# Performance work log

Measured on AMD Instinct MI355X. Metric: run time of the kernel, lower is better.

The kernel has to match this reference:

```python
import jax, jax.numpy as jnp
import numpy as np

KS = (3, 3)   # kernel_size
ST = (1, 1)   # stride
PD = (1, 1)   # padding
EPS = 1e-5


def unfold(x):
    """im2col matching torch.nn.Unfold: [B,C,H,W] -> [B, C*kh*kw, L] with (c,kh,kw) channel order, L row-major."""
    kh, kw = KS; sh, sw = ST; ph, pw = PD
    x = jnp.pad(x, ((0, 0), (0, 0), (ph, ph), (pw, pw)))
    B, C, H, W = x.shape
    Ho = (H - kh) // sh + 1
    Wo = (W - kw) // sw + 1
    I = (jnp.arange(Ho) * sh)[:, None, None, None] + jnp.arange(kh)[None, :, None, None]
    J = (jnp.arange(Wo) * sw)[None, None, :, None] + jnp.arange(kw)[None, None, None, :]
    p = x[:, :, I, J]  # [B, C, Ho, kh, Wo, kw]
    return p.transpose(0, 1, 3, 5, 2, 4).reshape(B, C * kh * kw, Ho * Wo)


def fold(cols, x_shape):
    """torch.nn.Fold is exactly the adjoint of Unfold (overlap-add)."""
    _, vjp = jax.vjp(unfold, jnp.zeros(x_shape, cols.dtype))
    return vjp(cols)[0]


def setup_inputs() -> dict:
    key = jax.random.key(0)
    k = jax.random.split(key, 6)
    B, C, H, W = 16, 64, 64, 64
    Cout, K = 64, KS[0] * KS[1]
    return {
        "x_mag": jax.random.uniform(k[0], (B, C, H, W), jnp.float32),
        "x_ang": jax.random.normal(k[1], (B, C, H, W), jnp.float32),
        "w_mag": jax.random.uniform(k[2], (C, K), jnp.float32),
        "w_ang": jax.random.uniform(k[3], (C, K), jnp.float32),
        "w1": jax.random.uniform(k[4], (C, K), jnp.float32),
        "w2": jax.random.uniform(k[5], (Cout, C), jnp.float32),
    }


def reference(x_mag, x_ang, w_mag, w_ang, w1, w2):
    B, C, H, W = x_mag.shape
    K = KS[0] * KS[1]
    Cout = w2.shape[0]
    Ho = (H + 2 * PD[0] - KS[0]) // ST[0] + 1
    Wo = (W + 2 * PD[1] - KS[1]) // ST[1] + 1

    # outer layer: unfold, mix with normalized weights, fold back (overlap-add)
    nws_mag = w_mag ** 2 / jnp.sum(w_mag ** 2)   # _normalize_weights_squared
    nw_ang = w_ang / jnp.sum(w_ang ** 2)         # _normalize_weights
    cm = unfold(x_mag).reshape(B, C, K, -1) + nws_mag[None, :, :, None]
    ca = unfold(x_ang).reshape(B, C, K, -1) * nw_ang[None, :, :, None]
    fm = fold(cm.reshape(B, C * K, -1), (B, C, H, W))
    fa = fold(ca.reshape(B, C * K, -1), (B, C, H, W))

    # helper: second unfold + weighted Frechet-mean reduction
    tbm = unfold(fm).reshape(B, C, K, -1)  # [B,C,K,L]
    tba = unfold(fa).reshape(B, C, K, -1)
    wmm1 = w1 ** 2 / jnp.sum(w1 ** 2, axis=1, keepdims=True)  # row-normalized
    wmm2 = w2 ** 2 / jnp.sum(w2 ** 2, axis=1, keepdims=True)
    wma1 = w1 ** 2 / jnp.sum(w1 ** 2)                          # globally normalized
    wma2 = w2 ** 2 / jnp.sum(w2 ** 2)

    m1 = jnp.einsum('bckl,ck->bcl', jnp.log(tbm + EPS), wmm1)
    out_mag = jnp.exp(jnp.einsum('bcl,oc->bol', m1, wmm2)).reshape(B, Cout, Ho, Wo)
    a1 = jnp.einsum('bckl,ck->bcl', tba, wma1)
    out_ang = jnp.einsum('bcl,oc->bol', a1, wma2).reshape(B, Cout, Ho, Wo)

    # from_polar -> stack (real, imag) on axis 1
    return jnp.stack([out_mag * jnp.cos(out_ang), out_mag * jnp.sin(out_ang)], axis=1)
```

## Files before the change

### kernel.cpp

```cpp
#include <hip/hip_runtime.h>
#include <math.h>

#define NB 16
#define NC 64
#define NL 4096
#define EPSF 1e-5f
#define LOG_EPSF -11.512925464970229f

#define WS_W2T   0
#define WS_RHO   4096
#define WS_CLS   4160
#define WS_WQ2   5312

#define FMA16(ACC, MV, W) \
  (ACC)[0].x = fmaf((MV).x,(W).x,(ACC)[0].x); (ACC)[0].y = fmaf((MV).y,(W).x,(ACC)[0].y); \
  (ACC)[0].z = fmaf((MV).z,(W).x,(ACC)[0].z); (ACC)[0].w = fmaf((MV).w,(W).x,(ACC)[0].w); \
  (ACC)[1].x = fmaf((MV).x,(W).y,(ACC)[1].x); (ACC)[1].y = fmaf((MV).y,(W).y,(ACC)[1].y); \
  (ACC)[1].z = fmaf((MV).z,(W).y,(ACC)[1].z); (ACC)[1].w = fmaf((MV).w,(W).y,(ACC)[1].w); \
  (ACC)[2].x = fmaf((MV).x,(W).z,(ACC)[2].x); (ACC)[2].y = fmaf((MV).y,(W).z,(ACC)[2].y); \
  (ACC)[2].z = fmaf((MV).z,(W).z,(ACC)[2].z); (ACC)[2].w = fmaf((MV).w,(W).z,(ACC)[2].w); \
  (ACC)[3].x = fmaf((MV).x,(W).w,(ACC)[3].x); (ACC)[3].y = fmaf((MV).y,(W).w,(ACC)[3].y); \
  (ACC)[3].z = fmaf((MV).z,(W).w,(ACC)[3].z); (ACC)[3].w = fmaf((MV).w,(W).w,(ACC)[3].w);

__global__ __launch_bounds__(256) void prep_kernel(
    const float* __restrict__ wm, const float* __restrict__ wa,
    const float* __restrict__ w1, const float* __restrict__ w2,
    float* __restrict__ ws)
{
    __shared__ float r2s[64];
    __shared__ float red[3][4];
    const int tid  = threadIdx.x;
    const int lane = tid & 63;
    const int wv   = tid >> 6;

    if (tid < 64) {
        float s = 0.f;
        for (int c = 0; c < 64; ++c) { float v = w2[tid * 64 + c]; s = fmaf(v, v, s); }
        r2s[tid] = s;
    }
    float p0 = 0.f, p1 = 0.f, p2 = 0.f;
    {
        float v;
        v = wm[tid]; p0 += v * v;  v = wm[tid + 256]; p0 += v * v;
        v = wa[tid]; p1 += v * v;  v = wa[tid + 256]; p1 += v * v;
        v = w1[tid]; p2 += v * v;  v = w1[tid + 256]; p2 += v * v;
        if (tid < 64) {
            v = wm[tid + 512]; p0 += v * v;
            v = wa[tid + 512]; p1 += v * v;
            v = w1[tid + 512]; p2 += v * v;
        }
    }
    #pragma unroll
    for (int s = 32; s; s >>= 1) {
        p0 += __shfl_down(p0, s); p1 += __shfl_down(p1, s); p2 += __shfl_down(p2, s);
    }
    if (lane == 0) { red[0][wv] = p0; red[1][wv] = p1; red[2][wv] = p2; }
    __syncthreads();
    const float s_wm2 = red[0][0] + red[0][1] + red[0][2] + red[0][3];
    const float s_wa2 = red[1][0] + red[1][1] + red[1][2] + red[1][3];
    const float s_w12 = red[2][0] + red[2][1] + red[2][2] + red[2][3];

    const int c0 = blockIdx.x * 4;
    {
        int c = c0 + (tid >> 6), o = tid & 63;
        float v = w2[o * 64 + c];
        ws[WS_W2T + c * 64 + o] = v * v / r2s[o];
    }

    if (blockIdx.x == 0) {
        if (tid < 64) {
            float s22 = 0.f;
            #pragma unroll
            for (int o = 0; o < 64; ++o) s22 += r2s[o];
            ws[WS_RHO + tid] = r2s[tid] / s22;

            const int c = tid;
            float nm[9], na[9];
            const float inv_m = 1.f / s_wm2, inv_a = 1.f / s_wa2;
            #pragma unroll
            for (int k = 0; k < 9; ++k) {
                float v = wm[c * 9 + k];
                nm[k] = v * v * inv_m;
                na[k] = wa[c * 9 + k] * inv_a;
            }
            #pragma unroll
            for (int ci_ = 0; ci_ < 3; ++ci_) {
                #pragma unroll
                for (int cj = 0; cj < 3; ++cj) {
                    float sm = 0.f, sa = 0.f;
                    #pragma unroll
                    for (int ki = 0; ki < 3; ++ki) {
                        bool vi = (ci_ == 0) ? (ki < 2) : ((ci_ == 2) ? (ki > 0) : true);
                        if (!vi) continue;
                        #pragma unroll
                        for (int kj = 0; kj < 3; ++kj) {
                            bool vj = (cj == 0) ? (kj < 2) : ((cj == 2) ? (kj > 0) : true);
                            if (!vj) continue;
                            sm += nm[ki * 3 + kj];
                            sa += na[ki * 3 + kj];
                        }
                    }
                    ws[WS_CLS + c * 9 + ci_ * 3 + cj] = sm;
                    ws[WS_CLS + 576 + c * 9 + ci_ * 3 + cj] = sa;
                }
            }
            float q[9]; float r1c = 0.f;
            #pragma unroll
            for (int k = 0; k < 9; ++k) { float v = w1[c * 9 + k]; q[k] = v * v; r1c += q[k]; }
            const float inv_r = 1.f / r1c, inv_s = 1.f / s_w12;
            #pragma unroll
            for (int k = 0; k < 9; ++k) {
                ws[WS_WQ2 + c * 18 + 2 * k]     = q[k] * inv_r;
                ws[WS_WQ2 + c * 18 + 2 * k + 1] = q[k] * inv_s;
            }
        }
    }
}

__global__ __launch_bounds__(256, 4) void fused_kernel(
    const float* __restrict__ x_mag, const float* __restrict__ x_ang,
    const float* __restrict__ ws, float* __restrict__ out)
{
    __shared__ float m1all[64][64];
    __shared__ float a1all[64][64];

    const int tid  = threadIdx.x;
    const int lane = tid & 63;
    const int wv   = tid >> 6;

    const int bid = (blockIdx.x & 7) * 128 + (blockIdx.x >> 3);
    const int b  = bid >> 6;
    const int iy = bid & 63;

    const int ir0 = iy - 1, ir2 = iy + 1;
    const bool ok0 = (ir0 >= 0), ok2 = (ir2 < 64);
    const int ci0 = (ir0 == 0) ? 0 : 1;
    const int ci1 = (iy == 0) ? 0 : ((iy == 63) ? 2 : 1);
    const int ci2 = (ir2 == 63) ? 2 : 1;
    const int ro0 = ok0 ? ir0 * 64 : 0;
    const int ro1 = iy * 64;
    const int ro2 = ok2 ? ir2 * 64 : 0;

    const bool e0  = (lane == 0);
    const bool e63 = (lane == 63);
    const bool edge = e0 | e63;

    const int cbase = wv * 16;
    const float* xmb = x_mag + ((size_t)(b * NC + cbase) * NL) + lane;
    const float* xab = x_ang + ((size_t)(b * NC + cbase) * NL) + lane;

    float pm[2][3], pa[2][3];
    {
        pm[0][0] = xmb[ro0]; pm[0][1] = xmb[ro1]; pm[0][2] = xmb[ro2];
        pa[0][0] = xab[ro0]; pa[0][1] = xab[ro1]; pa[0][2] = xab[ro2];
        pm[1][0] = xmb[NL + ro0]; pm[1][1] = xmb[NL + ro1]; pm[1][2] = xmb[NL + ro2];
        pa[1][0] = xab[NL + ro0]; pa[1][1] = xab[NL + ro1]; pa[1][2] = xab[NL + ro2];
    }

    #pragma unroll
    for (int t = 0; t < 16; ++t) {
        const int s = t & 1;
        const int cu = __builtin_amdgcn_readfirstlane(cbase + t);
        const float* clm = ws + WS_CLS + cu * 9;
        const float* cla = ws + WS_CLS + 576 + cu * 9;
        const float* qw  = ws + WS_WQ2 + cu * 18;

        float qm[9], qa[9];
        #pragma unroll
        for (int k = 0; k < 9; ++k) { qm[k] = qw[2 * k]; qa[k] = qw[2 * k + 1]; }

        float lm0, lm1, lm2, fa0, fa1, fa2;
        {
            float Sc = clm[ci1 * 3 + 1], Tc = cla[ci1 * 3 + 1];
            float S = e0 ? clm[ci1 * 3] : (e63 ? clm[ci1 * 3 + 2] : Sc);
            float T = e0 ? cla[ci1 * 3] : (e63 ? cla[ci1 * 3 + 2] : Tc);
            float ni = (ci1 == 1) ? 3.f : 2.f;
            float n = edge ? 2.f * ni : 3.f * ni;
            lm1 = __logf(fmaf(n, pm[s][1], S) + EPSF);
            fa1 = pa[s][1] * T;
        }
        if (ok0) {
            float Sc = clm[ci0 * 3 + 1], Tc = cla[ci0 * 3 + 1];
            float S = e0 ? clm[ci0 * 3] : (e63 ? clm[ci0 * 3 + 2] : Sc);
            float T = e0 ? cla[ci0 * 3] : (e63 ? cla[ci0 * 3 + 2] : Tc);
            float ni = (ci0 == 1) ? 3.f : 2.f;
            float n = edge ? 2.f * ni : 3.f * ni;
            lm0 = __logf(fmaf(n, pm[s][0], S) + EPSF);
            fa0 = pa[s][0] * T;
        } else { lm0 = LOG_EPSF; fa0 = 0.f; }
        if (ok2) {
            float Sc = clm[ci2 * 3 + 1], Tc = cla[ci2 * 3 + 1];
            float S = e0 ? clm[ci2 * 3] : (e63 ? clm[ci2 * 3 + 2] : Sc);
            float T = e0 ? cla[ci2 * 3] : (e63 ? cla[ci2 * 3 + 2] : Tc);
            float ni = (ci2 == 1) ? 3.f : 2.f;
            float n = edge ? 2.f * ni : 3.f * ni;
            lm2 = __logf(fmaf(n, pm[s][2], S) + EPSF);
            fa2 = pa[s][2] * T;
        } else { lm2 = LOG_EPSF; fa2 = 0.f; }

        if (t + 2 < 16) {
            const int off = (t + 2) * NL;
            pm[s][0] = xmb[off + ro0]; pm[s][1] = xmb[off + ro1]; pm[s][2] = xmb[off + ro2];
            pa[s][0] = xab[off + ro0]; pa[s][1] = xab[off + ro1]; pa[s][2] = xab[off + ro2];
        }

        float m1v, a1v;
        {
            float tm = qm[0] * lm0; tm = fmaf(qm[3], lm1, tm); tm = fmaf(qm[6], lm2, tm);
            float um = qm[1] * lm0; um = fmaf(qm[4], lm1, um); um = fmaf(qm[7], lm2, um);
            float vm = qm[2] * lm0; vm = fmaf(qm[5], lm1, vm); vm = fmaf(qm[8], lm2, vm);
            float sentL = LOG_EPSF * (qm[0] + qm[3] + qm[6]);
            float sentR = LOG_EPSF * (qm[2] + qm[5] + qm[8]);
            float tmL = __shfl_up(tm, 1);
            float vmR = __shfl_down(vm, 1);
            tmL = e0  ? sentL : tmL;
            vmR = e63 ? sentR : vmR;
            m1v = tmL + um + vmR;

            float ta = qa[0] * fa0; ta = fmaf(qa[3], fa1, ta); ta = fmaf(qa[6], fa2, ta);
            float ua = qa[1] * fa0; ua = fmaf(qa[4], fa1, ua); ua = fmaf(qa[7], fa2, ua);
            float va = qa[2] * fa0; va = fmaf(qa[5], fa1, va); va = fmaf(qa[8], fa2, va);
            float taL = __shfl_up(ta, 1);
            float vaR = __shfl_down(va, 1);
            taL = e0  ? 0.f : taL;
            vaR = e63 ? 0.f : vaR;
            a1v = taL + ua + vaR;
        }

        m1all[cbase + t][lane] = m1v;
        a1all[cbase + t][lane] = a1v;
    }

    __syncthreads();

    const int o0 = (tid >> 4) * 4;
    const int l0 = (tid & 15) * 4;
    const float* w2t_g = ws + WS_W2T;

    float4 accm[4], acca[4];
    #pragma unroll
    for (int oi = 0; oi < 4; ++oi) {
        accm[oi].x = accm[oi].y = accm[oi].z = accm[oi].w = 0.f;
        acca[oi].x = acca[oi].y = acca[oi].z = acca[oi].w = 0.f;
    }

    #pragma unroll 8
    for (int cc = 0; cc < 64; ++cc) {
        float4 w_ = *(const float4*)(w2t_g + (size_t)cc * 64 + o0);
        float4 mv = *(const float4*)&m1all[cc][l0];
        float4 av = *(const float4*)&a1all[cc][l0];
        FMA16(accm, mv, w_);
        FMA16(acca, av, w_);
    }

    {
        const float4 rh = *(const float4*)(ws + WS_RHO + o0);
        acca[0].x *= rh.x; acca[0].y *= rh.x; acca[0].z *= rh.x; acca[0].w *= rh.x;
        acca[1].x *= rh.y; acca[1].y *= rh.y; acca[1].z *= rh.y; acca[1].w *= rh.y;
        acca[2].x *= rh.z; acca[2].y *= rh.z; acca[2].z *= rh.z; acca[2].w *= rh.z;
        acca[3].x *= rh.w; acca[3].y *= rh.w; acca[3].z *= rh.w; acca[3].w *= rh.w;
    }

    #pragma unroll
    for (int oi = 0; oi < 4; ++oi) {
        float4 am = accm[oi], aa = acca[oi];
        float4 oc, os;
        float ex;
        ex = __expf(am.x); oc.x = ex * __cosf(aa.x); os.x = ex * __sinf(aa.x);
        ex = __expf(am.y); oc.y = ex * __cosf(aa.y); os.y = ex * __sinf(aa.y);
        ex = __expf(am.z); oc.z = ex * __cosf(aa.z); os.z = ex * __sinf(aa.z);
        ex = __expf(am.w); oc.w = ex * __cosf(aa.w); os.w = ex * __sinf(aa.w);
        size_t gi = ((size_t)(b * 2) * NC + o0 + oi) * NL + (size_t)iy * 64 + l0;
        *(float4*)&out[gi] = oc;
        *(float4*)&out[gi + (size_t)NC * NL] = os;
    }
}

extern "C" void kernel_launch(void* const* d_in, const int* in_sizes, int n_in,
                              void* d_out, int out_size, void* d_ws, size_t ws_size,
                              hipStream_t stream) {
    const float* x_mag = (const float*)d_in[0];
    const float* x_ang = (const float*)d_in[1];
    const float* w_mag = (const float*)d_in[2];
    const float* w_ang = (const float*)d_in[3];
    const float* w1    = (const float*)d_in[4];
    const float* w2    = (const float*)d_in[5];
    float* out = (float*)d_out;
    float* ws  = (float*)d_ws;

    prep_kernel<<<16, 256, 0, stream>>>(w_mag, w_ang, w1, w2, ws);
    fused_kernel<<<NB * 64, 256, 0, stream>>>(x_mag, x_ang, ws, out);
}
```

Measured before the change: 44.71 us.

## Double block size to 512 threads, halve per-thread channels and output tile, use packed FMA

```diff
diff --git a/kernel.cpp b/kernel.cpp
--- a/kernel.cpp
+++ b/kernel.cpp
@@ -11,16 +11,9 @@
 #define WS_RHO   4096
 #define WS_CLS   4160
 #define WS_WQ2   5312
-
-#define FMA16(ACC, MV, W) \
-  (ACC)[0].x = fmaf((MV).x,(W).x,(ACC)[0].x); (ACC)[0].y = fmaf((MV).y,(W).x,(ACC)[0].y); \
-  (ACC)[0].z = fmaf((MV).z,(W).x,(ACC)[0].z); (ACC)[0].w = fmaf((MV).w,(W).x,(ACC)[0].w); \
-  (ACC)[1].x = fmaf((MV).x,(W).y,(ACC)[1].x); (ACC)[1].y = fmaf((MV).y,(W).y,(ACC)[1].y); \
-  (ACC)[1].z = fmaf((MV).z,(W).y,(ACC)[1].z); (ACC)[1].w = fmaf((MV).w,(W).y,(ACC)[1].w); \
-  (ACC)[2].x = fmaf((MV).x,(W).z,(ACC)[2].x); (ACC)[2].y = fmaf((MV).y,(W).z,(ACC)[2].y); \
-  (ACC)[2].z = fmaf((MV).z,(W).z,(ACC)[2].z); (ACC)[2].w = fmaf((MV).w,(W).z,(ACC)[2].w); \
-  (ACC)[3].x = fmaf((MV).x,(W).w,(ACC)[3].x); (ACC)[3].y = fmaf((MV).y,(W).w,(ACC)[3].y); \
-  (ACC)[3].z = fmaf((MV).z,(W).w,(ACC)[3].z); (ACC)[3].w = fmaf((MV).w,(W).w,(ACC)[3].w);
+#define WS_SENT  6464
+
+typedef float f32x2 __attribute__((ext_vector_type(2)));
 
 __global__ __launch_bounds__(256) void prep_kernel(
     const float* __restrict__ wm, const float* __restrict__ wa,
@@ -113,11 +106,13 @@
                 ws[WS_WQ2 + c * 18 + 2 * k]     = q[k] * inv_r;
                 ws[WS_WQ2 + c * 18 + 2 * k + 1] = q[k] * inv_s;
             }
+            ws[WS_SENT + c * 2 + 0] = LOG_EPSF * (q[0] + q[3] + q[6]) * inv_r;
+            ws[WS_SENT + c * 2 + 1] = LOG_EPSF * (q[2] + q[5] + q[8]) * inv_r;
         }
     }
 }
 
-__global__ __launch_bounds__(256, 4) void fused_kernel(
+__global__ __launch_bounds__(512, 8) void fused_kernel(
     const float* __restrict__ x_mag, const float* __restrict__ x_ang,
     const float* __restrict__ ws, float* __restrict__ out)
 {
@@ -145,7 +140,7 @@
     const bool e63 = (lane == 63);
     const bool edge = e0 | e63;
 
-    const int cbase = wv * 16;
+    const int cbase = wv * 8;
     const float* xmb = x_mag + ((size_t)(b * NC + cbase) * NL) + lane;
     const float* xab = x_ang + ((size_t)(b * NC + cbase) * NL) + lane;
 
@@ -158,7 +153,7 @@
     }
 
     #pragma unroll
-    for (int t = 0; t < 16; ++t) {
+    for (int t = 0; t < 8; ++t) {
         const int s = t & 1;
         const int cu = __builtin_amdgcn_readfirstlane(cbase + t);
         const float* clm = ws + WS_CLS + cu * 9;
@@ -198,7 +193,7 @@
             fa2 = pa[s][2] * T;
         } else { lm2 = LOG_EPSF; fa2 = 0.f; }
 
-        if (t + 2 < 16) {
+        if (t + 2 < 8) {
             const int off = (t + 2) * NL;
             pm[s][0] = xmb[off + ro0]; pm[s][1] = xmb[off + ro1]; pm[s][2] = xmb[off + ro2];
             pa[s][0] = xab[off + ro0]; pa[s][1] = xab[off + ro1]; pa[s][2] = xab[off + ro2];
@@ -209,12 +204,10 @@
             float tm = qm[0] * lm0; tm = fmaf(qm[3], lm1, tm); tm = fmaf(qm[6], lm2, tm);
             float um = qm[1] * lm0; um = fmaf(qm[4], lm1, um); um = fmaf(qm[7], lm2, um);
             float vm = qm[2] * lm0; vm = fmaf(qm[5], lm1, vm); vm = fmaf(qm[8], lm2, vm);
-            float sentL = LOG_EPSF * (qm[0] + qm[3] + qm[6]);
-            float sentR = LOG_EPSF * (qm[2] + qm[5] + qm[8]);
             float tmL = __shfl_up(tm, 1);
             float vmR = __shfl_down(vm, 1);
-            tmL = e0  ? sentL : tmL;
-            vmR = e63 ? sentR : vmR;
+            tmL = e0  ? ws[WS_SENT + cu * 2 + 0] : tmL;
+            vmR = e63 ? ws[WS_SENT + cu * 2 + 1] : vmR;
             m1v = tmL + um + vmR;
 
             float ta = qa[0] * fa0; ta = fmaf(qa[3], fa1, ta); ta = fmaf(qa[6], fa2, ta);
@@ -233,46 +226,46 @@
 
     __syncthreads();
 
-    const int o0 = (tid >> 4) * 4;
-    const int l0 = (tid & 15) * 4;
+    const int o0 = (tid >> 5) * 4;
+    const int l0 = (tid & 31) * 2;
     const float* w2t_g = ws + WS_W2T;
 
-    float4 accm[4], acca[4];
-    #pragma unroll
-    for (int oi = 0; oi < 4; ++oi) {
-        accm[oi].x = accm[oi].y = accm[oi].z = accm[oi].w = 0.f;
-        acca[oi].x = acca[oi].y = acca[oi].z = acca[oi].w = 0.f;
-    }
+    f32x2 am4[4], aa4[4];
+    #pragma unroll
+    for (int oi = 0; oi < 4; ++oi) { am4[oi] = 0.f; aa4[oi] = 0.f; }
 
     #pragma unroll 8
     for (int cc = 0; cc < 64; ++cc) {
         float4 w_ = *(const float4*)(w2t_g + (size_t)cc * 64 + o0);
-        float4 mv = *(const float4*)&m1all[cc][l0];
-        float4 av = *(const float4*)&a1all[cc][l0];
-        FMA16(accm, mv, w_);
-        FMA16(acca, av, w_);
-    }
-
-    {
-        const float4 rh = *(const float4*)(ws + WS_RHO + o0);
-        acca[0].x *= rh.x; acca[0].y *= rh.x; acca[0].z *= rh.x; acca[0].w *= rh.x;
-        acca[1].x *= rh.y; acca[1].y *= rh.y; acca[1].z *= rh.y; acca[1].w *= rh.y;
-        acca[2].x *= rh.z; acca[2].y *= rh.z; acca[2].z *= rh.z; acca[2].w *= rh.z;
-        acca[3].x *= rh.w; acca[3].y *= rh.w; acca[3].z *= rh.w; acca[3].w *= rh.w;
+        f32x2 mv = *(const f32x2*)&m1all[cc][l0];
+        f32x2 av = *(const f32x2*)&a1all[cc][l0];
+        f32x2 w0; w0.x = w_.x; w0.y = w_.x;
+        f32x2 w1; w1.x = w_.y; w1.y = w_.y;
+        f32x2 w2s; w2s.x = w_.z; w2s.y = w_.z;
+        f32x2 w3; w3.x = w_.w; w3.y = w_.w;
+        am4[0] = __builtin_elementwise_fma(mv, w0, am4[0]);
+        am4[1] = __builtin_elementwise_fma(mv, w1, am4[1]);
+        am4[2] = __builtin_elementwise_fma(mv, w2s, am4[2]);
+        am4[3] = __builtin_elementwise_fma(mv, w3, am4[3]);
+        aa4[0] = __builtin_elementwise_fma(av, w0, aa4[0]);
+        aa4[1] = __builtin_elementwise_fma(av, w1, aa4[1]);
+        aa4[2] = __builtin_elementwise_fma(av, w2s, aa4[2]);
+        aa4[3] = __builtin_elementwise_fma(av, w3, aa4[3]);
     }
 
     #pragma unroll
     for (int oi = 0; oi < 4; ++oi) {
-        float4 am = accm[oi], aa = acca[oi];
-        float4 oc, os;
-        float ex;
-        ex = __expf(am.x); oc.x = ex * __cosf(aa.x); os.x = ex * __sinf(aa.x);
-        ex = __expf(am.y); oc.y = ex * __cosf(aa.y); os.y = ex * __sinf(aa.y);
-        ex = __expf(am.z); oc.z = ex * __cosf(aa.z); os.z = ex * __sinf(aa.z);
-        ex = __expf(am.w); oc.w = ex * __cosf(aa.w); os.w = ex * __sinf(aa.w);
-        size_t gi = ((size_t)(b * 2) * NC + o0 + oi) * NL + (size_t)iy * 64 + l0;
-        *(float4*)&out[gi] = oc;
-        *(float4*)&out[gi + (size_t)NC * NL] = os;
+        const int o = o0 + oi;
+        const float rho_o = ws[WS_RHO + o];
+        float amx = am4[oi].x, amy = am4[oi].y;
+        float aax = aa4[oi].x * rho_o, aay = aa4[oi].y * rho_o;
+        float exx = __expf(amx), exy = __expf(amy);
+        float2 oc, os;
+        oc.x = exx * __cosf(aax); os.x = exx * __sinf(aax);
+        oc.y = exy * __cosf(aay); os.y = exy * __sinf(aay);
+        size_t gi = ((size_t)(b * 2) * NC + o) * NL + (size_t)iy * 64 + l0;
+        *(float2*)&out[gi] = oc;
+        *(float2*)&out[gi + (size_t)NC * NL] = os;
     }
 }
 
@@ -289,5 +282,5 @@
     float* ws  = (float*)d_ws;
 
     prep_kernel<<<16, 256, 0, stream>>>(w_mag, w_ang, w1, w2, ws);
-    fused_kernel<<<NB * 64, 256, 0, stream>>>(x_mag, x_ang, ws, out);
+    fused_kernel<<<NB * 64, 512, 0, stream>>>(x_mag, x_ang, ws, out);
 }
```

Result: slower. 47.60 us (+6.5%).
